# Kernel optimization log

Measured on AMD Instinct MI355X. Metric: run time of the kernel, lower is better.

## Reference

```python
import jax, jax.numpy as jnp
import numpy as np

Q = 4096   # query_size = argument_size*relation_size*position_size = 32*16*8
L = 8192   # number of context rows


def setup_inputs() -> dict:
    key = jax.random.key(0)
    k1, k2, k3 = jax.random.split(key, 3)
    query = jax.random.normal(k1, (Q,), dtype=jnp.float32)
    context_vector = jax.random.normal(k2, (L, Q), dtype=jnp.float32)
    # torch Linear(2Q, Q, bias=False): weight shape [Q, 2Q], scaled init
    K_w = jax.random.normal(k3, (Q, 2 * Q), dtype=jnp.float32) / np.sqrt(2 * Q)
    return {"query": query, "context_vector": context_vector, "K_w": K_w}


def reference(query, context_vector, K_w):
    # score[l] = <context_vector[l], query>  -> [L]
    score = context_vector @ query
    attention = jax.nn.softmax(score, axis=0)          # softmax over L
    s_t = attention @ context_vector                    # [Q]
    gamma = jnp.concatenate([query, s_t])               # [2Q]
    return K_w @ gamma                                   # Linear(2Q -> Q), no bias
```

## Files before the change

### kernel.cpp

```cpp
#include <hip/hip_runtime.h>

#define Q 4096
#define L 8192

__global__ __launch_bounds__(256) void k1_kernel(
    const float* __restrict__ qvec, const float* __restrict__ ctx,
    const float* __restrict__ Kw, float* __restrict__ score,
    float* __restrict__ out1)
{
    const int b   = blockIdx.x;
    const int fam = b % 3;
    const int g   = b / 3;
    const int tid  = threadIdx.x;
    const int lane = tid & 63;
    const int wid  = tid >> 6;

    const float4* __restrict__ row;
    float* outp;
    if (fam < 2) {
        const int l = g * 2 + fam;
        row  = (const float4*)(ctx + (size_t)l * Q);
        outp = score + l;
    } else {
        row  = (const float4*)(Kw + (size_t)g * (2 * Q));
        outp = out1 + g;
    }

    const float4* __restrict__ qv = (const float4*)qvec;
    float acc = 0.f;
    #pragma unroll
    for (int i = tid; i < Q / 4; i += 256) {
        float4 a = row[i];
        float4 c = qv[i];
        acc = fmaf(a.x, c.x, acc);
        acc = fmaf(a.y, c.y, acc);
        acc = fmaf(a.z, c.z, acc);
        acc = fmaf(a.w, c.w, acc);
    }
    #pragma unroll
    for (int off = 32; off > 0; off >>= 1) acc += __shfl_down(acc, off, 64);

    __shared__ float red[4];
    if (lane == 0) red[wid] = acc;
    __syncthreads();
    if (tid == 0) *outp = red[0] + red[1] + red[2] + red[3];
}

__global__ __launch_bounds__(1024) void softmax_kernel(
    const float* __restrict__ score, float* __restrict__ att)
{
    __shared__ float redm[16];
    __shared__ float reds[16];
    const int tid  = threadIdx.x;
    const int lane = tid & 63;
    const int wid  = tid >> 6;

    float m = -3.4e38f;
    for (int i = tid; i < L; i += 1024) m = fmaxf(m, score[i]);
    #pragma unroll
    for (int off = 32; off > 0; off >>= 1) m = fmaxf(m, __shfl_down(m, off, 64));
    if (lane == 0) redm[wid] = m;
    __syncthreads();
    float M = redm[0];
    #pragma unroll
    for (int w = 1; w < 16; ++w) M = fmaxf(M, redm[w]);

    float s = 0.f;
    for (int i = tid; i < L; i += 1024) s += __expf(score[i] - M);
    #pragma unroll
    for (int off = 32; off > 0; off >>= 1) s += __shfl_down(s, off, 64);
    if (lane == 0) reds[wid] = s;
    __syncthreads();
    float Z = 0.f;
    #pragma unroll
    for (int w = 0; w < 16; ++w) Z += reds[w];
    const float inv = 1.0f / Z;

    for (int i = tid; i < L; i += 1024) att[i] = __expf(score[i] - M) * inv;
}

__global__ __launch_bounds__(256) void wsum_kernel(
    const float* __restrict__ ctx, const float* __restrict__ att,
    float* __restrict__ partial)
{
    __shared__ float att_s[128];
    const int cc = blockIdx.x & 7;
    const int rc = blockIdx.x >> 3;
    const int tid = threadIdx.x;
    const int rg  = tid >> 7;
    const int col = cc * 128 + (tid & 127);

    if (tid < 128) att_s[tid] = att[rc * 128 + tid];
    __syncthreads();

    const float4* __restrict__ cb = (const float4*)ctx;
    const int r0 = rc * 128 + rg * 64;
    float4 acc = make_float4(0.f, 0.f, 0.f, 0.f);
    #pragma unroll 8
    for (int r = 0; r < 64; ++r) {
        const float a = att_s[rg * 64 + r];
        float4 v = cb[(size_t)(r0 + r) * (Q / 4) + col];
        acc.x = fmaf(a, v.x, acc.x);
        acc.y = fmaf(a, v.y, acc.y);
        acc.z = fmaf(a, v.z, acc.z);
        acc.w = fmaf(a, v.w, acc.w);
    }
    ((float4*)partial)[(size_t)(rc * 2 + rg) * (Q / 4) + col] = acc;
}

__global__ __launch_bounds__(256) void reduce_kernel(
    const float* __restrict__ partial, float* __restrict__ s_t)
{
    const int c4 = blockIdx.x * 256 + threadIdx.x;
    const float4* __restrict__ p = (const float4*)partial;
    float4 acc = make_float4(0.f, 0.f, 0.f, 0.f);
    #pragma unroll 8
    for (int b = 0; b < 128; ++b) {
        float4 v = p[(size_t)b * (Q / 4) + c4];
        acc.x += v.x; acc.y += v.y; acc.z += v.z; acc.w += v.w;
    }
    ((float4*)s_t)[c4] = acc;
}

__global__ __launch_bounds__(256) void k5_kernel(
    const float* __restrict__ Kw, const float* __restrict__ s_t,
    const float* __restrict__ out1, float* __restrict__ out)
{
    const int i = blockIdx.x;
    const int tid  = threadIdx.x;
    const int lane = tid & 63;
    const int wid  = tid >> 6;
    const float4* __restrict__ row = (const float4*)(Kw + (size_t)i * (2 * Q) + Q);
    const float4* __restrict__ sv  = (const float4*)s_t;

    float acc = 0.f;
    #pragma unroll
    for (int j = tid; j < Q / 4; j += 256) {
        float4 a = row[j];
        float4 c = sv[j];
        acc = fmaf(a.x, c.x, acc);
        acc = fmaf(a.y, c.y, acc);
        acc = fmaf(a.z, c.z, acc);
        acc = fmaf(a.w, c.w, acc);
    }
    #pragma unroll
    for (int off = 32; off > 0; off >>= 1) acc += __shfl_down(acc, off, 64);

    __shared__ float red[4];
    if (lane == 0) red[wid] = acc;
    __syncthreads();
    if (tid == 0) out[i] = out1[i] + red[0] + red[1] + red[2] + red[3];
}

extern "C" void kernel_launch(void* const* d_in, const int* in_sizes, int n_in,
                              void* d_out, int out_size, void* d_ws, size_t ws_size,
                              hipStream_t stream)
{
    const float* query = (const float*)d_in[0];
    const float* ctx   = (const float*)d_in[1];
    const float* Kw    = (const float*)d_in[2];
    float* out = (float*)d_out;

    float* ws      = (float*)d_ws;
    float* score   = ws;
    float* att     = ws + L;
    float* out1    = ws + 2 * L;
    float* s_t     = ws + 2 * L + Q;
    float* partial = ws + 2 * L + 2 * Q;

    k1_kernel<<<12288, 256, 0, stream>>>(query, ctx, Kw, score, out1);
    softmax_kernel<<<1, 1024, 0, stream>>>(score, att);
    wsum_kernel<<<512, 256, 0, stream>>>(ctx, att, partial);
    reduce_kernel<<<4, 256, 0, stream>>>(partial, s_t);
    k5_kernel<<<Q, 256, 0, stream>>>(Kw, s_t, out1, out);
}
```

Before: 79.86 us.

## Use wave-per-row dot products and move Kw query half into output kernel

```diff
diff --git a/kernel.cpp b/kernel.cpp
--- a/kernel.cpp
+++ b/kernel.cpp
@@ -3,47 +3,35 @@
 #define Q 4096
 #define L 8192
 
-__global__ __launch_bounds__(256) void k1_kernel(
-    const float* __restrict__ qvec, const float* __restrict__ ctx,
-    const float* __restrict__ Kw, float* __restrict__ score,
-    float* __restrict__ out1)
+__global__ __launch_bounds__(256) void score_kernel(
+    const float* __restrict__ ctx, const float* __restrict__ qvec,
+    float* __restrict__ score)
 {
-    const int b   = blockIdx.x;
-    const int fam = b % 3;
-    const int g   = b / 3;
-    const int tid  = threadIdx.x;
-    const int lane = tid & 63;
-    const int wid  = tid >> 6;
+    const int lane = threadIdx.x & 63;
+    const int w    = blockIdx.x * 4 + (threadIdx.x >> 6);
+    const float4* __restrict__ row = (const float4*)(ctx + (size_t)w * Q);
+    const float4* __restrict__ qv  = (const float4*)qvec;
 
-    const float4* __restrict__ row;
-    float* outp;
-    if (fam < 2) {
-        const int l = g * 2 + fam;
-        row  = (const float4*)(ctx + (size_t)l * Q);
-        outp = score + l;
-    } else {
-        row  = (const float4*)(Kw + (size_t)g * (2 * Q));
-        outp = out1 + g;
+    float a0 = 0.f, a1 = 0.f, a2 = 0.f, a3 = 0.f;
+    #pragma unroll
+    for (int c = 0; c < 16; c += 4) {
+        float4 x0 = row[(c + 0) * 64 + lane], y0 = qv[(c + 0) * 64 + lane];
+        float4 x1 = row[(c + 1) * 64 + lane], y1 = qv[(c + 1) * 64 + lane];
+        float4 x2 = row[(c + 2) * 64 + lane], y2 = qv[(c + 2) * 64 + lane];
+        float4 x3 = row[(c + 3) * 64 + lane], y3 = qv[(c + 3) * 64 + lane];
+        a0 = fmaf(x0.x, y0.x, a0); a0 = fmaf(x0.y, y0.y, a0);
+        a0 = fmaf(x0.z, y0.z, a0); a0 = fmaf(x0.w, y0.w, a0);
+        a1 = fmaf(x1.x, y1.x, a1); a1 = fmaf(x1.y, y1.y, a1);
+        a1 = fmaf(x1.z, y1.z, a1); a1 = fmaf(x1.w, y1.w, a1);
+        a2 = fmaf(x2.x, y2.x, a2); a2 = fmaf(x2.y, y2.y, a2);
+        a2 = fmaf(x2.z, y2.z, a2); a2 = fmaf(x2.w, y2.w, a2);
+        a3 = fmaf(x3.x, y3.x, a3); a3 = fmaf(x3.y, y3.y, a3);
+        a3 = fmaf(x3.z, y3.z, a3); a3 = fmaf(x3.w, y3.w, a3);
     }
-
-    const float4* __restrict__ qv = (const float4*)qvec;
-    float acc = 0.f;
+    float d = (a0 + a1) + (a2 + a3);
     #pragma unroll
-    for (int i = tid; i < Q / 4; i += 256) {
-        float4 a = row[i];
-        float4 c = qv[i];
-        acc = fmaf(a.x, c.x, acc);
-        acc = fmaf(a.y, c.y, acc);
-        acc = fmaf(a.z, c.z, acc);
-        acc = fmaf(a.w, c.w, acc);
-    }
-    #pragma unroll
-    for (int off = 32; off > 0; off >>= 1) acc += __shfl_down(acc, off, 64);
-
-    __shared__ float red[4];
-    if (lane == 0) red[wid] = acc;
-    __syncthreads();
-    if (tid == 0) *outp = red[0] + red[1] + red[2] + red[3];
+    for (int off = 32; off > 0; off >>= 1) d += __shfl_down(d, off, 64);
+    if (lane == 0) score[w] = d;
 }
 
 __global__ __launch_bounds__(1024) void softmax_kernel(
@@ -83,29 +71,28 @@
     const float* __restrict__ ctx, const float* __restrict__ att,
     float* __restrict__ partial)
 {
-    __shared__ float att_s[128];
-    const int cc = blockIdx.x & 7;
-    const int rc = blockIdx.x >> 3;
+    __shared__ float att_s[64];
+    const int cc  = blockIdx.x & 3;
+    const int rc  = blockIdx.x >> 2;
     const int tid = threadIdx.x;
-    const int rg  = tid >> 7;
-    const int col = cc * 128 + (tid & 127);
+    const int col = cc * 256 + tid;
 
-    if (tid < 128) att_s[tid] = att[rc * 128 + tid];
+    if (tid < 64) att_s[tid] = att[rc * 64 + tid];
     __syncthreads();
 
     const float4* __restrict__ cb = (const float4*)ctx;
-    const int r0 = rc * 128 + rg * 64;
+    const int r0 = rc * 64;
     float4 acc = make_float4(0.f, 0.f, 0.f, 0.f);
     #pragma unroll 8
     for (int r = 0; r < 64; ++r) {
-        const float a = att_s[rg * 64 + r];
+        const float a = att_s[r];
         float4 v = cb[(size_t)(r0 + r) * (Q / 4) + col];
         acc.x = fmaf(a, v.x, acc.x);
         acc.y = fmaf(a, v.y, acc.y);
         acc.z = fmaf(a, v.z, acc.z);
         acc.w = fmaf(a, v.w, acc.w);
     }
-    ((float4*)partial)[(size_t)(rc * 2 + rg) * (Q / 4) + col] = acc;
+    ((float4*)partial)[(size_t)rc * (Q / 4) + col] = acc;
 }
 
 __global__ __launch_bounds__(256) void reduce_kernel(
@@ -122,34 +109,51 @@
     ((float4*)s_t)[c4] = acc;
 }
 
-__global__ __launch_bounds__(256) void k5_kernel(
-    const float* __restrict__ Kw, const float* __restrict__ s_t,
-    const float* __restrict__ out1, float* __restrict__ out)
+__global__ __launch_bounds__(256) void out_kernel(
+    const float* __restrict__ Kw, const float* __restrict__ qvec,
+    const float* __restrict__ s_t, float* __restrict__ out)
 {
-    const int i = blockIdx.x;
-    const int tid  = threadIdx.x;
-    const int lane = tid & 63;
-    const int wid  = tid >> 6;
-    const float4* __restrict__ row = (const float4*)(Kw + (size_t)i * (2 * Q) + Q);
+    const int lane = threadIdx.x & 63;
+    const int i    = blockIdx.x * 4 + (threadIdx.x >> 6);
+    const float4* __restrict__ row = (const float4*)(Kw + (size_t)i * (2 * Q));
+    const float4* __restrict__ qv  = (const float4*)qvec;
     const float4* __restrict__ sv  = (const float4*)s_t;
 
-    float acc = 0.f;
+    float a0 = 0.f, a1 = 0.f, a2 = 0.f, a3 = 0.f;
     #pragma unroll
-    for (int j = tid; j < Q / 4; j += 256) {
-        float4 a = row[j];
-        float4 c = sv[j];
-        acc = fmaf(a.x, c.x, acc);
-        acc = fmaf(a.y, c.y, acc);
-        acc = fmaf(a.z, c.z, acc);
-        acc = fmaf(a.w, c.w, acc);
+    for (int c = 0; c < 16; c += 4) {
+        float4 x0 = row[(c + 0) * 64 + lane], y0 = qv[(c + 0) * 64 + lane];
+        float4 x1 = row[(c + 1) * 64 + lane], y1 = qv[(c + 1) * 64 + lane];
+        float4 x2 = row[(c + 2) * 64 + lane], y2 = qv[(c + 2) * 64 + lane];
+        float4 x3 = row[(c + 3) * 64 + lane], y3 = qv[(c + 3) * 64 + lane];
+        a0 = fmaf(x0.x, y0.x, a0); a0 = fmaf(x0.y, y0.y, a0);
+        a0 = fmaf(x0.z, y0.z, a0); a0 = fmaf(x0.w, y0.w, a0);
+        a1 = fmaf(x1.x, y1.x, a1); a1 = fmaf(x1.y, y1.y, a1);
+        a1 = fmaf(x1.z, y1.z, a1); a1 = fmaf(x1.w, y1.w, a1);
+        a2 = fmaf(x2.x, y2.x, a2); a2 = fmaf(x2.y, y2.y, a2);
+        a2 = fmaf(x2.z, y2.z, a2); a2 = fmaf(x2.w, y2.w, a2);
+        a3 = fmaf(x3.x, y3.x, a3); a3 = fmaf(x3.y, y3.y, a3);
+        a3 = fmaf(x3.z, y3.z, a3); a3 = fmaf(x3.w, y3.w, a3);
     }
     #pragma unroll
-    for (int off = 32; off > 0; off >>= 1) acc += __shfl_down(acc, off, 64);
-
-    __shared__ float red[4];
-    if (lane == 0) red[wid] = acc;
-    __syncthreads();
-    if (tid == 0) out[i] = out1[i] + red[0] + red[1] + red[2] + red[3];
+    for (int c = 0; c < 16; c += 4) {
+        float4 x0 = row[(16 + c + 0) * 64 + lane], y0 = sv[(c + 0) * 64 + lane];
+        float4 x1 = row[(16 + c + 1) * 64 + lane], y1 = sv[(c + 1) * 64 + lane];
+        float4 x2 = row[(16 + c + 2) * 64 + lane], y2 = sv[(c + 2) * 64 + lane];
+        float4 x3 = row[(16 + c + 3) * 64 + lane], y3 = sv[(c + 3) * 64 + lane];
+        a0 = fmaf(x0.x, y0.x, a0); a0 = fmaf(x0.y, y0.y, a0);
+        a0 = fmaf(x0.z, y0.z, a0); a0 = fmaf(x0.w, y0.w, a0);
+        a1 = fmaf(x1.x, y1.x, a1); a1 = fmaf(x1.y, y1.y, a1);
+        a1 = fmaf(x1.z, y1.z, a1); a1 = fmaf(x1.w, y1.w, a1);
+        a2 = fmaf(x2.x, y2.x, a2); a2 = fmaf(x2.y, y2.y, a2);
+        a2 = fmaf(x2.z, y2.z, a2); a2 = fmaf(x2.w, y2.w, a2);
+        a3 = fmaf(x3.x, y3.x, a3); a3 = fmaf(x3.y, y3.y, a3);
+        a3 = fmaf(x3.z, y3.z, a3); a3 = fmaf(x3.w, y3.w, a3);
+    }
+    float d = (a0 + a1) + (a2 + a3);
+    #pragma unroll
+    for (int off = 32; off > 0; off >>= 1) d += __shfl_down(d, off, 64);
+    if (lane == 0) out[i] = d;
 }
 
 extern "C" void kernel_launch(void* const* d_in, const int* in_sizes, int n_in,
@@ -164,13 +168,12 @@
     float* ws      = (float*)d_ws;
     float* score   = ws;
     float* att     = ws + L;
-    float* out1    = ws + 2 * L;
-    float* s_t     = ws + 2 * L + Q;
-    float* partial = ws + 2 * L + 2 * Q;
+    float* s_t     = ws + 2 * L;
+    float* partial = ws + 2 * L + Q;
 
-    k1_kernel<<<12288, 256, 0, stream>>>(query, ctx, Kw, score, out1);
+    score_kernel<<<2048, 256, 0, stream>>>(ctx, query, score);
     softmax_kernel<<<1, 1024, 0, stream>>>(score, att);
     wsum_kernel<<<512, 256, 0, stream>>>(ctx, att, partial);
     reduce_kernel<<<4, 256, 0, stream>>>(partial, s_t);
-    k5_kernel<<<Q, 256, 0, stream>>>(Kw, s_t, out1, out);
+    out_kernel<<<1024, 256, 0, stream>>>(Kw, query, s_t, out);
 }
```

After: 83.16 us. +4.1%, slower.
